# Optimization experiments

Measured on AMD Instinct MI355X. Metric: run time of the kernel, lower is better.

Reference implementation:

```python
import jax, jax.numpy as jnp
import numpy as np

THRESHOLD = 6.2
N_SECTIONS = 9      # n_conv_sections
SEC_LEN = 4         # n_section_length
SEC_H = 9           # n_input_sections + n_section_length - 1
BATCH = 16384


def setup_inputs() -> dict:
    key = jax.random.key(0)
    k1, k2 = jax.random.split(key)
    # input spike-wave tensor [T, C=1, H=41, W=40]
    x = jax.random.uniform(k1, (BATCH, 1, 41, 40), dtype=jnp.float32)
    # per-section conv weights, N(0.8, 0.05) as in snn.Convolution init
    W = 0.8 + 0.05 * jax.random.normal(k2, (N_SECTIONS, 50, 1, 6, 40), dtype=jnp.float32)
    return {"x": x, "W": W}


def _conv(sec, w):
    # sec: [B,1,9,40], w: [50,1,6,40] -> [B,50,4,1]
    return jax.lax.conv_general_dilated(
        sec, w, window_strides=(1, 1), padding='VALID',
        dimension_numbers=('NCHW', 'OIHW', 'NCHW'))


def reference(x, W):
    # slice the 9 overlapping input sections -> [9, B, 1, 9, 40]
    sec = jnp.stack([x[:, :, i * SEC_LEN:i * SEC_LEN + SEC_H, :]
                     for i in range(N_SECTIONS)])
    pots = jax.vmap(_conv)(sec, W)                      # [9, B, 50, 4, 1]
    pots = jnp.max(pots, axis=3, keepdims=True)         # Pooling((4,1)) -> [9, B, 50, 1, 1]
    spks = jnp.where(pots > THRESHOLD, 1.0, 0.0).astype(pots.dtype)
    # concat sections along height (dim=2 of [B,C,H,W])
    pots_cat = jnp.moveaxis(pots[:, :, :, 0, :], 0, 2)  # [B, 50, 9, 1]
    spks_cat = jnp.moveaxis(spks[:, :, :, 0, :], 0, 2)  # [B, 50, 9, 1]
    return pots_cat, spks_cat
```

## Files before the change

### kernel.cpp

```cpp
#include <hip/hip_runtime.h>
#include <cstdint>
#include <cstddef>

#define NBATCH   16384
#define NSEC     9
#define NOC      50
#define NOCP     64
#define KREAL    240
#define KPAD     256
#define XROW     1640
#define XS2      1672
#define TB       16
#define OUTHALF  7372800
#define THRESH   6.2f

typedef _Float16 half8  __attribute__((ext_vector_type(8)));
typedef _Float16 half4v __attribute__((ext_vector_type(4)));
typedef float    f32x4  __attribute__((ext_vector_type(4)));

__global__ __launch_bounds__(256)
void wconv_kernel(const float* __restrict__ W, _Float16* __restrict__ wks) {
    int idx = blockIdx.x * 256 + threadIdx.x;
    int k   = idx & 255;
    int ocp = (idx >> 8) & 63;
    int sec = idx >> 14;
    float v = 0.0f;
    if (ocp < NOC && k < KREAL)
        v = W[(size_t)(sec * NOC + ocp) * KREAL + k];
    wks[idx] = (_Float16)v;
}

__global__ __launch_bounds__(256, 3)
void fused_kernel(const float* __restrict__ x,
                  const _Float16* __restrict__ wks,
                  float* __restrict__ out) {
    __shared__ __align__(16) _Float16 xs[TB * XS2];

    const int tid = threadIdx.x;
    const size_t b0 = (size_t)blockIdx.x * TB;

    if (tid < 32) {
        half8 z = {};
        int b = tid >> 1, off = XROW + (tid & 1) * 8;
        *(half8*)&xs[b * XS2 + off] = z;
    }

    const float* xg = x + b0 * XROW;
    for (int c = tid; c < TB * 410; c += 256) {
        int b = c / 410, cc = c - b * 410;
        float4 v = *(const float4*)(xg + (size_t)b * XROW + cc * 4);
        half4v h;
        h.x = (_Float16)v.x; h.y = (_Float16)v.y;
        h.z = (_Float16)v.z; h.w = (_Float16)v.w;
        *(half4v*)&xs[b * XS2 + cc * 4] = h;
    }
    __syncthreads();

    const int lane = tid & 63;
    const int w    = tid >> 6;
    const int l15  = lane & 15;
    const int quad = lane >> 4;

    const _Float16* xrow = xs + l15 * XS2 + quad * 8;
    const _Float16* wrow = wks + (size_t)(w * 16 + l15) * KPAD + quad * 8;

    f32x4 res[NSEC];

    for (int s = 0; s < NSEC; ++s) {
        const _Float16* wsec = wrow + (size_t)s * (NOCP * KPAD);
        half8 bv[8];
        #pragma unroll
        for (int kk = 0; kk < 8; ++kk)
            bv[kk] = *(const half8*)(wsec + kk * 32);

        f32x4 acc[4] = {f32x4{}, f32x4{}, f32x4{}, f32x4{}};
        const _Float16* xsec = xrow + s * 160;
        #pragma unroll
        for (int kk = 0; kk < 8; ++kk) {
            #pragma unroll
            for (int h = 0; h < 4; ++h) {
                half8 av = *(const half8*)(xsec + h * 40 + kk * 32);
                acc[h] = __builtin_amdgcn_mfma_f32_16x16x32_f16(
                             av, bv[kk], acc[h], 0, 0, 0);
            }
        }
        f32x4 r;
        #pragma unroll
        for (int j = 0; j < 4; ++j)
            r[j] = fmaxf(fmaxf(acc[0][j], acc[1][j]),
                         fmaxf(acc[2][j], acc[3][j]));
        res[s] = r;
    }

    __syncthreads();
    float* t = (float*)xs;
    const int oc = w * 16 + l15;
    if (oc < NOC) {
        #pragma unroll
        for (int s = 0; s < NSEC; ++s)
            #pragma unroll
            for (int r = 0; r < 4; ++r)
                t[(quad * 4 + r) * 450 + oc * 9 + s] = res[s][r];
    }
    __syncthreads();

    const size_t ob = b0 * 450;
    for (int i = tid; i < TB * 450; i += 256) {
        float v = t[i];
        out[ob + i] = v;
        out[OUTHALF + ob + i] = (v > THRESH) ? 1.0f : 0.0f;
    }
}

__global__ __launch_bounds__(256)
void naive_kernel(const float* __restrict__ x, const float* __restrict__ W,
                  float* __restrict__ out) {
    size_t idx = (size_t)blockIdx.x * 256 + threadIdx.x;
    if (idx >= OUTHALF) return;
    int s  = (int)(idx % NSEC);
    int oc = (int)((idx / NSEC) % NOC);
    int b  = (int)(idx / (NSEC * NOC));
    const float* xb = x + (size_t)b * XROW + s * 160;
    const float* wv = W + (size_t)(s * NOC + oc) * KREAL;
    float best = -1e30f;
    for (int h0 = 0; h0 < 4; ++h0) {
        float acc = 0.0f;
        for (int k = 0; k < KREAL; ++k)
            acc += xb[h0 * 40 + k] * wv[k];
        best = fmaxf(best, acc);
    }
    out[idx] = best;
    out[OUTHALF + idx] = (best > THRESH) ? 1.0f : 0.0f;
}

extern "C" void kernel_launch(void* const* d_in, const int* in_sizes, int n_in,
                              void* d_out, int out_size, void* d_ws, size_t ws_size,
                              hipStream_t stream) {
    const float* x = (const float*)d_in[0];
    const float* W = (const float*)d_in[1];
    float* out = (float*)d_out;

    const size_t w_bytes = (size_t)NSEC * NOCP * KPAD * sizeof(_Float16);

    if (ws_size < w_bytes) {
        naive_kernel<<<(OUTHALF + 255) / 256, 256, 0, stream>>>(x, W, out);
        return;
    }

    _Float16* wks = (_Float16*)d_ws;

    wconv_kernel<<<(NSEC * NOCP * KPAD) / 256, 256, 0, stream>>>(W, wks);
    fused_kernel<<<NBATCH / TB, 256, 0, stream>>>(x, wks, out);
}
```

Baseline: 236.7 us.

## XOR-swizzle LDS input rows and batch global loads for MLP

Reorganizes the input staging so each thread loads a row's 16-byte units with many outstanding float4 loads, converts them to half8, and stores them into shared memory at XOR-swizzled unit positions. The MFMA A-operand reads apply the same swizzle, aiming to remove LDS bank conflicts from the padded-stride layout. The explicit zero-padding writes are replaced by zero-filling out-of-range units. It adds index arithmetic and register pressure from holding 14 float4 values at once.

```diff
diff --git a/kernel.cpp b/kernel.cpp
--- a/kernel.cpp
+++ b/kernel.cpp
@@ -6,16 +6,16 @@
 #define NSEC     9
 #define NOC      50
 #define NOCP     64
+#define KPAD     256
 #define KREAL    240
-#define KPAD     256
 #define XROW     1640
-#define XS2      1672
+#define XUNITS   208
+#define XSF      1664
 #define TB       16
 #define OUTHALF  7372800
 #define THRESH   6.2f
 
 typedef _Float16 half8  __attribute__((ext_vector_type(8)));
-typedef _Float16 half4v __attribute__((ext_vector_type(4)));
 typedef float    f32x4  __attribute__((ext_vector_type(4)));
 
 __global__ __launch_bounds__(256)
@@ -34,25 +34,48 @@
 void fused_kernel(const float* __restrict__ x,
                   const _Float16* __restrict__ wks,
                   float* __restrict__ out) {
-    __shared__ __align__(16) _Float16 xs[TB * XS2];
+    __shared__ __align__(16) _Float16 xs[TB * XSF];
 
     const int tid = threadIdx.x;
     const size_t b0 = (size_t)blockIdx.x * TB;
 
-    if (tid < 32) {
-        half8 z = {};
-        int b = tid >> 1, off = XROW + (tid & 1) * 8;
-        *(half8*)&xs[b * XS2 + off] = z;
-    }
+    {
+        const int bb  = tid >> 4;
+        const int u16 = tid & 15;
+        const int sw  = bb & 7;
+        const float* xrow = x + (b0 + bb) * XROW;
+        _Float16* lrow = xs + bb * XSF;
 
-    const float* xg = x + b0 * XROW;
-    for (int c = tid; c < TB * 410; c += 256) {
-        int b = c / 410, cc = c - b * 410;
-        float4 v = *(const float4*)(xg + (size_t)b * XROW + cc * 4);
-        half4v h;
-        h.x = (_Float16)v.x; h.y = (_Float16)v.y;
-        h.z = (_Float16)v.z; h.w = (_Float16)v.w;
-        *(half4v*)&xs[b * XS2 + cc * 4] = h;
+        #pragma unroll
+        for (int c = 0; c < 2; ++c) {
+            const int jn = c ? 6 : 7;
+            float4 va[7], vb[7];
+            #pragma unroll
+            for (int jj = 0; jj < 7; ++jj) {
+                if (jj < jn) {
+                    int u = u16 + 16 * (c * 7 + jj);
+                    if (u < 205) {
+                        va[jj] = *(const float4*)(xrow + u * 8);
+                        vb[jj] = *(const float4*)(xrow + u * 8 + 4);
+                    } else {
+                        va[jj] = float4{0, 0, 0, 0};
+                        vb[jj] = float4{0, 0, 0, 0};
+                    }
+                }
+            }
+            #pragma unroll
+            for (int jj = 0; jj < 7; ++jj) {
+                if (jj < jn) {
+                    int u = u16 + 16 * (c * 7 + jj);
+                    half8 h;
+                    h[0] = (_Float16)va[jj].x; h[1] = (_Float16)va[jj].y;
+                    h[2] = (_Float16)va[jj].z; h[3] = (_Float16)va[jj].w;
+                    h[4] = (_Float16)vb[jj].x; h[5] = (_Float16)vb[jj].y;
+                    h[6] = (_Float16)vb[jj].z; h[7] = (_Float16)vb[jj].w;
+                    *(half8*)(lrow + ((u ^ sw) << 3)) = h;
+                }
+            }
+        }
     }
     __syncthreads();
 
@@ -60,8 +83,9 @@
     const int w    = tid >> 6;
     const int l15  = lane & 15;
     const int quad = lane >> 4;
+    const int sw   = l15 & 7;
 
-    const _Float16* xrow = xs + l15 * XS2 + quad * 8;
+    const _Float16* arow = xs + l15 * XSF;
     const _Float16* wrow = wks + (size_t)(w * 16 + l15) * KPAD + quad * 8;
 
     f32x4 res[NSEC];
@@ -74,12 +98,13 @@
             bv[kk] = *(const half8*)(wsec + kk * 32);
 
         f32x4 acc[4] = {f32x4{}, f32x4{}, f32x4{}, f32x4{}};
-        const _Float16* xsec = xrow + s * 160;
+        const int su = s * 20 + quad;
         #pragma unroll
         for (int kk = 0; kk < 8; ++kk) {
             #pragma unroll
             for (int h = 0; h < 4; ++h) {
-                half8 av = *(const half8*)(xsec + h * 40 + kk * 32);
+                int unit = su + h * 5 + kk * 4;
+                half8 av = *(const half8*)(arow + ((unit ^ sw) << 3));
                 acc[h] = __builtin_amdgcn_mfma_f32_16x16x32_f16(
                              av, bv[kk], acc[h], 0, 0, 0);
             }
```

Measured after the change: 216.1 us. 8.7% less time.

## Load activations directly from global and split sections across waves with 4x4 MFMA tiles

Applied to the files above, without the earlier changes.

The kernel no longer stages the input batch tile in shared memory. Each lane loads fp32 activations straight from global memory and converts them with packed round-to-zero conversion. Work is split so each wave handles two sections across all 64 padded output channels, which lets A fragments be reused across four B tiles. Section 8 is shared across waves by output-channel group, and results are held as fp16 before being written out as float4 stores. This removes the LDS staging and its barrier, at the cost of redundant global reads of x across waves, more register pressure, and fp16 rounding of the stored potentials, which could flip spikes near the threshold.

```diff
diff --git a/kernel.cpp b/kernel.cpp
--- a/kernel.cpp
+++ b/kernel.cpp
@@ -6,20 +6,23 @@
 #define NSEC     9
 #define NOC      50
 #define NOCP     64
+#define KPAD     256
 #define KREAL    240
-#define KPAD     256
 #define XROW     1640
-#define XS2      1672
 #define TB       16
+#define WELEMS   147456
+#define WBLOCKS  576
 #define OUTHALF  7372800
 #define THRESH   6.2f
 
 typedef _Float16 half8  __attribute__((ext_vector_type(8)));
 typedef _Float16 half4v __attribute__((ext_vector_type(4)));
+typedef __fp16   fp16x2 __attribute__((ext_vector_type(2)));
+typedef __fp16   fp16x8 __attribute__((ext_vector_type(8)));
 typedef float    f32x4  __attribute__((ext_vector_type(4)));
 
 __global__ __launch_bounds__(256)
-void wconv_kernel(const float* __restrict__ W, _Float16* __restrict__ wks) {
+void wprep_kernel(const float* __restrict__ W, _Float16* __restrict__ wks) {
     int idx = blockIdx.x * 256 + threadIdx.x;
     int k   = idx & 255;
     int ocp = (idx >> 8) & 63;
@@ -30,85 +33,131 @@
     wks[idx] = (_Float16)v;
 }
 
+__device__ __forceinline__ half8 load_a8(const float* __restrict__ p) {
+    float4 a = *(const float4*)p;
+    float4 b = *(const float4*)(p + 4);
+    fp16x2 c0 = __builtin_amdgcn_cvt_pkrtz(a.x, a.y);
+    fp16x2 c1 = __builtin_amdgcn_cvt_pkrtz(a.z, a.w);
+    fp16x2 c2 = __builtin_amdgcn_cvt_pkrtz(b.x, b.y);
+    fp16x2 c3 = __builtin_amdgcn_cvt_pkrtz(b.z, b.w);
+    fp16x8 r;
+    r[0] = c0[0]; r[1] = c0[1]; r[2] = c1[0]; r[3] = c1[1];
+    r[4] = c2[0]; r[5] = c2[1]; r[6] = c3[0]; r[7] = c3[1];
+    return __builtin_bit_cast(half8, r);
+}
+
 __global__ __launch_bounds__(256, 3)
-void fused_kernel(const float* __restrict__ x,
-                  const _Float16* __restrict__ wks,
-                  float* __restrict__ out) {
-    __shared__ __align__(16) _Float16 xs[TB * XS2];
-
-    const int tid = threadIdx.x;
-    const size_t b0 = (size_t)blockIdx.x * TB;
-
-    if (tid < 32) {
-        half8 z = {};
-        int b = tid >> 1, off = XROW + (tid & 1) * 8;
-        *(half8*)&xs[b * XS2 + off] = z;
-    }
-
-    const float* xg = x + b0 * XROW;
-    for (int c = tid; c < TB * 410; c += 256) {
-        int b = c / 410, cc = c - b * 410;
-        float4 v = *(const float4*)(xg + (size_t)b * XROW + cc * 4);
-        half4v h;
-        h.x = (_Float16)v.x; h.y = (_Float16)v.y;
-        h.z = (_Float16)v.z; h.w = (_Float16)v.w;
-        *(half4v*)&xs[b * XS2 + cc * 4] = h;
-    }
-    __syncthreads();
-
+void fused2_kernel(const float* __restrict__ x,
+                   const _Float16* __restrict__ wks,
+                   float* __restrict__ out) {
+    __shared__ float t[TB * 450];
+
+    const int tid  = threadIdx.x;
     const int lane = tid & 63;
     const int w    = tid >> 6;
     const int l15  = lane & 15;
     const int quad = lane >> 4;
-
-    const _Float16* xrow = xs + l15 * XS2 + quad * 8;
-    const _Float16* wrow = wks + (size_t)(w * 16 + l15) * KPAD + quad * 8;
-
-    f32x4 res[NSEC];
-
-    for (int s = 0; s < NSEC; ++s) {
-        const _Float16* wsec = wrow + (size_t)s * (NOCP * KPAD);
-        half8 bv[8];
-        #pragma unroll
-        for (int kk = 0; kk < 8; ++kk)
-            bv[kk] = *(const half8*)(wsec + kk * 32);
-
+    const int b0   = blockIdx.x * TB;
+
+    const float* __restrict__ ar = x + (size_t)(b0 + l15) * XROW;
+
+    half4v res[2][4];
+    half4v res8;
+
+    #pragma unroll
+    for (int si = 0; si < 2; ++si) {
+        const int s = 2 * w + si;
+        const _Float16* __restrict__ wp =
+            wks + ((size_t)s * NOCP + l15) * KPAD + quad * 8;
+        f32x4 acc[4][4] = {};
+        #pragma unroll
+        for (int kk = 0; kk < 8; ++kk) {
+            half8 av[4], bv[4];
+            #pragma unroll
+            for (int h = 0; h < 4; ++h) {
+                int off = s * 160 + h * 40 + kk * 32 + quad * 8;
+                av[h] = load_a8(ar + off);
+            }
+            #pragma unroll
+            for (int n = 0; n < 4; ++n)
+                bv[n] = *(const half8*)(wp + n * 16 * KPAD + kk * 32);
+            #pragma unroll
+            for (int h = 0; h < 4; ++h)
+                #pragma unroll
+                for (int n = 0; n < 4; ++n)
+                    acc[h][n] = __builtin_amdgcn_mfma_f32_16x16x32_f16(
+                                    av[h], bv[n], acc[h][n], 0, 0, 0);
+        }
+        #pragma unroll
+        for (int n = 0; n < 4; ++n) {
+            half4v r;
+            #pragma unroll
+            for (int j = 0; j < 4; ++j)
+                r[j] = (_Float16)fmaxf(fmaxf(acc[0][n][j], acc[1][n][j]),
+                                       fmaxf(acc[2][n][j], acc[3][n][j]));
+            res[si][n] = r;
+        }
+    }
+
+    {
+        const _Float16* __restrict__ wp =
+            wks + ((size_t)8 * NOCP + w * 16 + l15) * KPAD + quad * 8;
         f32x4 acc[4] = {f32x4{}, f32x4{}, f32x4{}, f32x4{}};
-        const _Float16* xsec = xrow + s * 160;
         #pragma unroll
         for (int kk = 0; kk < 8; ++kk) {
+            half8 bv = *(const half8*)(wp + kk * 32);
             #pragma unroll
             for (int h = 0; h < 4; ++h) {
-                half8 av = *(const half8*)(xsec + h * 40 + kk * 32);
+                int off = 8 * 160 + h * 40 + kk * 32 + quad * 8;
+                if (off > XROW - 8) off = XROW - 8;
+                half8 av = load_a8(ar + off);
                 acc[h] = __builtin_amdgcn_mfma_f32_16x16x32_f16(
-                             av, bv[kk], acc[h], 0, 0, 0);
+                             av, bv, acc[h], 0, 0, 0);
             }
         }
-        f32x4 r;
+        half4v r;
         #pragma unroll
         for (int j = 0; j < 4; ++j)
-            r[j] = fmaxf(fmaxf(acc[0][j], acc[1][j]),
-                         fmaxf(acc[2][j], acc[3][j]));
-        res[s] = r;
-    }
-
+            r[j] = (_Float16)fmaxf(fmaxf(acc[0][j], acc[1][j]),
+                                   fmaxf(acc[2][j], acc[3][j]));
+        res8 = r;
+    }
+
+    #pragma unroll
+    for (int si = 0; si < 2; ++si) {
+        const int s = 2 * w + si;
+        #pragma unroll
+        for (int n = 0; n < 4; ++n) {
+            const int oc = n * 16 + l15;
+            if (oc < NOC) {
+                #pragma unroll
+                for (int j = 0; j < 4; ++j)
+                    t[(quad * 4 + j) * 450 + oc * 9 + s] = (float)res[si][n][j];
+            }
+        }
+    }
+    {
+        const int oc = w * 16 + l15;
+        if (oc < NOC) {
+            #pragma unroll
+            for (int j = 0; j < 4; ++j)
+                t[(quad * 4 + j) * 450 + oc * 9 + 8] = (float)res8[j];
+        }
+    }
     __syncthreads();
-    float* t = (float*)xs;
-    const int oc = w * 16 + l15;
-    if (oc < NOC) {
-        #pragma unroll
-        for (int s = 0; s < NSEC; ++s)
-            #pragma unroll
-            for (int r = 0; r < 4; ++r)
-                t[(quad * 4 + r) * 450 + oc * 9 + s] = res[s][r];
-    }
-    __syncthreads();
-
-    const size_t ob = b0 * 450;
-    for (int i = tid; i < TB * 450; i += 256) {
-        float v = t[i];
-        out[ob + i] = v;
-        out[OUTHALF + ob + i] = (v > THRESH) ? 1.0f : 0.0f;
+
+    const size_t ob4 = (size_t)blockIdx.x * (TB * 450 / 4);
+    float4* __restrict__ o4 = (float4*)out;
+    float4* __restrict__ s4 = (float4*)(out + OUTHALF);
+    for (int i = tid; i < TB * 450 / 4; i += 256) {
+        float4 v = ((const float4*)t)[i];
+        o4[ob4 + i] = v;
+        float4 sp;
+        sp.x = (v.x > THRESH) ? 1.0f : 0.0f;
+        sp.y = (v.y > THRESH) ? 1.0f : 0.0f;
+        sp.z = (v.z > THRESH) ? 1.0f : 0.0f;
+        sp.w = (v.w > THRESH) ? 1.0f : 0.0f;
+        s4[ob4 + i] = sp;
     }
 }
 
@@ -140,7 +189,7 @@
     const float* W = (const float*)d_in[1];
     float* out = (float*)d_out;
 
-    const size_t w_bytes = (size_t)NSEC * NOCP * KPAD * sizeof(_Float16);
+    const size_t w_bytes = (size_t)WELEMS * sizeof(_Float16);
 
     if (ws_size < w_bytes) {
         naive_kernel<<<(OUTHALF + 255) / 256, 256, 0, stream>>>(x, W, out);
@@ -148,7 +197,6 @@
     }
 
     _Float16* wks = (_Float16*)d_ws;
-
-    wconv_kernel<<<(NSEC * NOCP * KPAD) / 256, 256, 0, stream>>>(W, wks);
-    fused_kernel<<<NBATCH / TB, 256, 0, stream>>>(x, wks, out);
-}
+    wprep_kernel<<<WBLOCKS, 256, 0, stream>>>(W, wks);
+    fused2_kernel<<<NBATCH / TB, 256, 0, stream>>>(x, wks, out);
+}
```

After: 292.4 us. +23.5%, slower.
